# Optimization experiments

Hardware: AMD Instinct MI355X
Metric: run time of the kernel (lower is better)

Reference implementation:

```python
import jax, jax.numpy as jnp
import numpy as np
import math

SAMPLE_RATE = 16000
CUTOFF = 7500.0
Q = 0.707  # torchaudio default for lowpass_biquad

def _lowpass_biquad_coeffs(sample_rate, cutoff_freq, Q):
    w0 = 2.0 * math.pi * cutoff_freq / sample_rate
    alpha = math.sin(w0) / (2.0 * Q)
    cos_w0 = math.cos(w0)
    b0 = (1.0 - cos_w0) / 2.0
    b1 = 1.0 - cos_w0
    b2 = b0
    a0 = 1.0 + alpha
    a1 = -2.0 * cos_w0
    a2 = 1.0 - alpha
    # normalize by a0 (as torchaudio's biquad/lfilter does)
    return (b0 / a0, b1 / a0, b2 / a0, a1 / a0, a2 / a0)


def setup_inputs() -> dict:
    key = jax.random.key(0)
    x = jax.random.normal(key, (64, 320000), dtype=jnp.float32)
    return {"x": x}


def reference(x) -> jnp.ndarray:
    b0, b1, b2, a1, a2 = _lowpass_biquad_coeffs(SAMPLE_RATE, CUTOFF, Q)
    b0 = jnp.asarray(b0, x.dtype); b1 = jnp.asarray(b1, x.dtype)
    b2 = jnp.asarray(b2, x.dtype); a1 = jnp.asarray(a1, x.dtype)
    a2 = jnp.asarray(a2, x.dtype)

    B = x.shape[0]
    xT = jnp.swapaxes(x, 0, 1)  # [T, B] -> scan over time

    def step(carry, xn):
        x1, x2, y1, y2 = carry  # each [B]
        yn = b0 * xn + b1 * x1 + b2 * x2 - a1 * y1 - a2 * y2
        return (xn, x1, yn, y1), yn

    z = jnp.zeros((B,), x.dtype)
    _, yT = jax.lax.scan(step, (z, z, z, z), xT)
    return jnp.swapaxes(yT, 0, 1)  # [B, T]
```

## Files before the change

kernel.cpp:

```cpp
#include <hip/hip_runtime.h>
#include <cmath>

#ifndef M_PI
#define M_PI 3.14159265358979323846
#endif

constexpr int T_LEN  = 320000;
constexpr int B_ROWS = 64;
constexpr int CHUNK  = 32;
constexpr int VPT    = CHUNK / 4;
constexpr int NCHUNK = T_LEN / CHUNK;
constexpr int BLK_CHUNKS = 128;
constexpr int BLK_SPAN   = BLK_CHUNKS * CHUNK;
constexpr int HALO       = 3;
constexpr int HALO_VECS  = HALO * VPT;
constexpr int TILE_VECS  = HALO_VECS + BLK_CHUNKS * VPT;

__device__ __forceinline__ int swzv(int V) { return V ^ ((V >> 3) & 7); }

__global__ __launch_bounds__(256, 8) void biquad_combine_kernel(
    const float* __restrict__ x, float* __restrict__ y,
    float b0, float b1, float b2, float a1, float a2,
    float q30, float p30, float q31, float p31) {
  const int b   = blockIdx.x;
  const int row = blockIdx.y;
  const int t   = threadIdx.x;

  const int S       = b * BLK_SPAN;
  const int nchunks = min(BLK_CHUNKS, (T_LEN - S) / CHUNK);
  const int nvecs   = nchunks * VPT;

  const float* xr = x + (size_t)row * T_LEN;
  float*       yr = y + (size_t)row * T_LEN;

  __shared__ float4 tile[TILE_VECS];
  __shared__ float4 st[HALO + BLK_CHUNKS];

  if (b == 0) {
    const float4* src = reinterpret_cast<const float4*>(xr);
    for (int i = t; i < HALO_VECS + nvecs; i += 256)
      tile[swzv(i)] = (i < HALO_VECS) ? make_float4(0.f, 0.f, 0.f, 0.f)
                                      : src[i - HALO_VECS];
  } else {
    const float4* src = reinterpret_cast<const float4*>(xr + S - HALO * CHUNK);
    for (int i = t; i < HALO_VECS + nvecs; i += 256) tile[swzv(i)] = src[i];
  }
  __syncthreads();

  auto stepf = [&](float xn, float& X1, float& X2, float& Y1, float& Y2) -> float {
    float tt = fmaf(b2, X2, fmaf(b1, X1, b0 * xn));
    float u  = fmaf(-a2, Y2, tt);
    float yn = fmaf(-a1, Y1, u);
    X2 = X1; X1 = xn;
    Y2 = Y1; Y1 = yn;
    return yn;
  };

  if (t < HALO) {
    float4 h[VPT];
#pragma unroll
    for (int k = 0; k < VPT; ++k) h[k] = tile[swzv(t * VPT + k)];
    float hxl1 = h[VPT - 1].w, hxl2 = h[VPT - 1].z;
    float hx1 = 0.f, hx2 = 0.f, hy1 = 0.f, hy2 = 0.f;
#pragma unroll
    for (int k = 0; k < VPT; ++k) {
      stepf(h[k].x, hx1, hx2, hy1, hy2); stepf(h[k].y, hx1, hx2, hy1, hy2);
      stepf(h[k].z, hx1, hx2, hy1, hy2); stepf(h[k].w, hx1, hx2, hy1, hy2);
    }
    st[t] = make_float4(hy1, hy2, hxl1, hxl2);
  }

  const bool active = (t < nchunks);
  float4 m[VPT];
  const int vb = HALO_VECS + t * VPT;
  if (active) {
#pragma unroll
    for (int k = 0; k < VPT; ++k) m[k] = tile[swzv(vb + k)];
    float xl1 = m[VPT - 1].w, xl2 = m[VPT - 1].z;
    float x1 = 0.f, x2 = 0.f, y1 = 0.f, y2 = 0.f;
#pragma unroll
    for (int k = 0; k < VPT; ++k) {
      float4 v = m[k];
      m[k] = make_float4(stepf(v.x, x1, x2, y1, y2), stepf(v.y, x1, x2, y1, y2),
                         stepf(v.z, x1, x2, y1, y2), stepf(v.w, x1, x2, y1, y2));
    }
    st[HALO + t] = make_float4(y1, y2, xl1, xl2);
  }
  __syncthreads();

  if (active) {
    const int i = HALO + t;
    float4 sm3 = st[i - 3], sm2 = st[i - 2], sm1 = st[i - 1];
    float cA0 = fmaf(b1, sm3.z, fmaf(b2, sm3.w, fmaf(-a1, sm3.x, -a2 * sm3.y)));
    float cA1 = fmaf(-a1, cA0, fmaf(b2, sm3.z, -a2 * sm3.x));
    float yA1 = fmaf(q31, cA0, fmaf(p31, cA1, sm2.x));
    float yA2 = fmaf(q30, cA0, fmaf(p30, cA1, sm2.y));
    float cB0 = fmaf(b1, sm2.z, fmaf(b2, sm2.w, fmaf(-a1, yA1, -a2 * yA2)));
    float cB1 = fmaf(-a1, cB0, fmaf(b2, sm2.z, -a2 * yA1));
    float yB1 = fmaf(q31, cB0, fmaf(p31, cB1, sm1.x));
    float yB2 = fmaf(q30, cB0, fmaf(p30, cB1, sm1.y));
    float c0 = fmaf(b1, sm1.z, fmaf(b2, sm1.w, fmaf(-a1, yB1, -a2 * yB2)));
    float c1 = fmaf(-a1, c0, fmaf(b2, sm1.z, -a2 * yB1));
    float cm2, cm1;
    {
      m[0].x += c0; m[0].y += c1;
      float c2 = fmaf(-a1, c1, -a2 * c0); m[0].z += c2;
      float c3 = fmaf(-a1, c2, -a2 * c1); m[0].w += c3;
      cm2 = c2; cm1 = c3;
    }
#pragma unroll
    for (int k = 1; k < VPT; ++k) {
      float ca = fmaf(-a1, cm1, -a2 * cm2); m[k].x += ca;
      float cb = fmaf(-a1, ca, -a2 * cm1);  m[k].y += cb;
      float cc = fmaf(-a1, cb, -a2 * ca);   m[k].z += cc;
      float cd = fmaf(-a1, cc, -a2 * cb);   m[k].w += cd;
      cm2 = cc; cm1 = cd;
    }
#pragma unroll
    for (int k = 0; k < VPT; ++k) tile[swzv(vb + k)] = m[k];
  }
  __syncthreads();

  {
    float4* dst = reinterpret_cast<float4*>(yr + S);
    for (int i = t; i < nvecs; i += 256) dst[i] = tile[swzv(HALO_VECS + i)];
  }
}

extern "C" void kernel_launch(void* const* d_in, const int* in_sizes, int n_in,
                              void* d_out, int out_size, void* d_ws, size_t ws_size,
                              hipStream_t stream) {
  const float* x = (const float*)d_in[0];
  float*       y = (float*)d_out;

  const double sample_rate = 16000.0, cutoff = 7500.0, Q = 0.707;
  double w0    = 2.0 * M_PI * cutoff / sample_rate;
  double alpha = sin(w0) / (2.0 * Q);
  double cw    = cos(w0);
  double a0    = 1.0 + alpha;
  double b0d = ((1.0 - cw) * 0.5) / a0;
  double b1d = (1.0 - cw) / a0;
  double a1d = (-2.0 * cw) / a0;
  double a2d = (1.0 - alpha) / a0;

  double qm2 = 1.0, pm2 = 0.0, qm1 = 0.0, pm1 = 1.0;
  double q30 = 0, p30 = 0, q31 = 0, p31 = 0;
  for (int n = 2; n < CHUNK; ++n) {
    double qn = -a1d * qm1 - a2d * qm2;
    double pn = -a1d * pm1 - a2d * pm2;
    qm2 = qm1; pm2 = pm1; qm1 = qn; pm1 = pn;
    if (n == 30) { q30 = qn; p30 = pn; }
    if (n == 31) { q31 = qn; p31 = pn; }
  }

  dim3 block(256);
  dim3 grid((NCHUNK + BLK_CHUNKS - 1) / BLK_CHUNKS, B_ROWS);
  hipLaunchKernelGGL(biquad_combine_kernel, grid, block, 0, stream,
                     x, y, (float)b0d, (float)b1d, (float)b0d, (float)a1d, (float)a2d,
                     (float)q30, (float)p30, (float)q31, (float)p31);
}
```

Before: 33.71 us.

## Exchange chunk carry states via wavefront shuffles instead of shared memory

Each thread's end-of-chunk state (y1, y2, last two inputs) now reaches its neighbours through 64-lane shuffles rather than a shared-memory array and an extra block barrier. Every wavefront computes its own three-chunk halo so lane 0 can take its neighbours' state from broadcasts. The global load is unrolled into five register loads issued before any LDS store, and the occupancy hint in launch_bounds drops from 8 to 4. The intent is to remove a __syncthreads and LDS round-trips and to get more loads in flight. The cost is redundant halo work in every wave, and threads 128–255 now read LDS beyond the tile unguarded (only their stores are guarded).

```diff
diff --git a/kernel.cpp b/kernel.cpp
--- a/kernel.cpp
+++ b/kernel.cpp
@@ -18,32 +18,61 @@
 
 __device__ __forceinline__ int swzv(int V) { return V ^ ((V >> 3) & 7); }
 
-__global__ __launch_bounds__(256, 8) void biquad_combine_kernel(
+__device__ __forceinline__ float4 shfl_up4(float4 v, int d) {
+  float4 r;
+  r.x = __shfl_up(v.x, d); r.y = __shfl_up(v.y, d);
+  r.z = __shfl_up(v.z, d); r.w = __shfl_up(v.w, d);
+  return r;
+}
+__device__ __forceinline__ float4 bcast4(float4 v, int l) {
+  float4 r;
+  r.x = __shfl(v.x, l); r.y = __shfl(v.y, l);
+  r.z = __shfl(v.z, l); r.w = __shfl(v.w, l);
+  return r;
+}
+
+__global__ __launch_bounds__(256, 4) void biquad_shfl_kernel(
     const float* __restrict__ x, float* __restrict__ y,
     float b0, float b1, float b2, float a1, float a2,
     float q30, float p30, float q31, float p31) {
-  const int b   = blockIdx.x;
-  const int row = blockIdx.y;
-  const int t   = threadIdx.x;
+  const int b    = blockIdx.x;
+  const int row  = blockIdx.y;
+  const int t    = threadIdx.x;
+  const int lane = t & 63;
 
   const int S       = b * BLK_SPAN;
   const int nchunks = min(BLK_CHUNKS, (T_LEN - S) / CHUNK);
   const int nvecs   = nchunks * VPT;
+  const int ntot    = HALO_VECS + nvecs;
 
   const float* xr = x + (size_t)row * T_LEN;
   float*       yr = y + (size_t)row * T_LEN;
 
   __shared__ float4 tile[TILE_VECS];
-  __shared__ float4 st[HALO + BLK_CHUNKS];
-
-  if (b == 0) {
-    const float4* src = reinterpret_cast<const float4*>(xr);
-    for (int i = t; i < HALO_VECS + nvecs; i += 256)
-      tile[swzv(i)] = (i < HALO_VECS) ? make_float4(0.f, 0.f, 0.f, 0.f)
-                                      : src[i - HALO_VECS];
-  } else {
-    const float4* src = reinterpret_cast<const float4*>(xr + S - HALO * CHUNK);
-    for (int i = t; i < HALO_VECS + nvecs; i += 256) tile[swzv(i)] = src[i];
+
+  {
+    const float4 z4 = make_float4(0.f, 0.f, 0.f, 0.f);
+    float4 v0, v1, v2, v3, v4;
+    if (b == 0) {
+      const float4* g = reinterpret_cast<const float4*>(xr);
+      v0 = (t >= HALO_VECS && t < ntot) ? g[t - HALO_VECS] : z4;
+      v1 = (t + 256  < ntot) ? g[t + 256  - HALO_VECS] : z4;
+      v2 = (t + 512  < ntot) ? g[t + 512  - HALO_VECS] : z4;
+      v3 = (t + 768  < ntot) ? g[t + 768  - HALO_VECS] : z4;
+      v4 = (t + 1024 < ntot) ? g[t + 1024 - HALO_VECS] : z4;
+    } else {
+      const float4* g = reinterpret_cast<const float4*>(xr + S - HALO * CHUNK);
+      v0 = (t        < ntot) ? g[t]        : z4;
+      v1 = (t + 256  < ntot) ? g[t + 256]  : z4;
+      v2 = (t + 512  < ntot) ? g[t + 512]  : z4;
+      v3 = (t + 768  < ntot) ? g[t + 768]  : z4;
+      v4 = (t + 1024 < ntot) ? g[t + 1024] : z4;
+    }
+    if (t        < ntot) tile[swzv(t)]        = v0;
+    if (t + 256  < ntot) tile[swzv(t + 256)]  = v1;
+    if (t + 512  < ntot) tile[swzv(t + 512)]  = v2;
+    if (t + 768  < ntot) tile[swzv(t + 768)]  = v3;
+    if (t + 1024 < ntot) tile[swzv(t + 1024)] = v4;
   }
   __syncthreads();
 
@@ -56,27 +85,29 @@
     return yn;
   };
 
-  if (t < HALO) {
-    float4 h[VPT];
-#pragma unroll
-    for (int k = 0; k < VPT; ++k) h[k] = tile[swzv(t * VPT + k)];
-    float hxl1 = h[VPT - 1].w, hxl2 = h[VPT - 1].z;
-    float hx1 = 0.f, hx2 = 0.f, hy1 = 0.f, hy2 = 0.f;
-#pragma unroll
-    for (int k = 0; k < VPT; ++k) {
-      stepf(h[k].x, hx1, hx2, hy1, hy2); stepf(h[k].y, hx1, hx2, hy1, hy2);
-      stepf(h[k].z, hx1, hx2, hy1, hy2); stepf(h[k].w, hx1, hx2, hy1, hy2);
-    }
-    st[t] = make_float4(hy1, hy2, hxl1, hxl2);
-  }
-
-  const bool active = (t < nchunks);
+  float4 H = make_float4(0.f, 0.f, 0.f, 0.f);
+  if (lane < 3) {
+    const int hvb = HALO_VECS + ((t & ~63) - 3 + lane) * VPT;
+    float hx1 = 0.f, hx2 = 0.f, hy1 = 0.f, hy2 = 0.f, hxl1 = 0.f, hxl2 = 0.f;
+#pragma unroll
+    for (int g2 = 0; g2 < 4; ++g2) {
+      float4 ha = tile[swzv(hvb + 2 * g2)];
+      float4 hb = tile[swzv(hvb + 2 * g2 + 1)];
+      stepf(ha.x, hx1, hx2, hy1, hy2); stepf(ha.y, hx1, hx2, hy1, hy2);
+      stepf(ha.z, hx1, hx2, hy1, hy2); stepf(ha.w, hx1, hx2, hy1, hy2);
+      stepf(hb.x, hx1, hx2, hy1, hy2); stepf(hb.y, hx1, hx2, hy1, hy2);
+      stepf(hb.z, hx1, hx2, hy1, hy2); stepf(hb.w, hx1, hx2, hy1, hy2);
+      if (g2 == 3) { hxl1 = hb.w; hxl2 = hb.z; }
+    }
+    H = make_float4(hy1, hy2, hxl1, hxl2);
+  }
+
   float4 m[VPT];
   const int vb = HALO_VECS + t * VPT;
-  if (active) {
-#pragma unroll
-    for (int k = 0; k < VPT; ++k) m[k] = tile[swzv(vb + k)];
-    float xl1 = m[VPT - 1].w, xl2 = m[VPT - 1].z;
+#pragma unroll
+  for (int k = 0; k < VPT; ++k) m[k] = tile[swzv(vb + k)];
+  float xl1 = m[VPT - 1].w, xl2 = m[VPT - 1].z;
+  {
     float x1 = 0.f, x2 = 0.f, y1 = 0.f, y2 = 0.f;
 #pragma unroll
     for (int k = 0; k < VPT; ++k) {
@@ -84,13 +115,15 @@
       m[k] = make_float4(stepf(v.x, x1, x2, y1, y2), stepf(v.y, x1, x2, y1, y2),
                          stepf(v.z, x1, x2, y1, y2), stepf(v.w, x1, x2, y1, y2));
     }
-    st[HALO + t] = make_float4(y1, y2, xl1, xl2);
-  }
-  __syncthreads();
-
-  if (active) {
-    const int i = HALO + t;
-    float4 sm3 = st[i - 3], sm2 = st[i - 2], sm1 = st[i - 1];
+    float4 Sst = make_float4(y1, y2, xl1, xl2);
+    float4 up1 = shfl_up4(Sst, 1);
+    float4 up2 = shfl_up4(Sst, 2);
+    float4 up3 = shfl_up4(Sst, 3);
+    float4 H0 = bcast4(H, 0), H1 = bcast4(H, 1), H2 = bcast4(H, 2);
+    float4 sm1 = (lane == 0) ? H2 : up1;
+    float4 sm2 = (lane == 0) ? H1 : ((lane == 1) ? H2 : up2);
+    float4 sm3 = (lane == 0) ? H0 : ((lane == 1) ? H1 : ((lane == 2) ? H2 : up3));
+
     float cA0 = fmaf(b1, sm3.z, fmaf(b2, sm3.w, fmaf(-a1, sm3.x, -a2 * sm3.y)));
     float cA1 = fmaf(-a1, cA0, fmaf(b2, sm3.z, -a2 * sm3.x));
     float yA1 = fmaf(q31, cA0, fmaf(p31, cA1, sm2.x));
@@ -116,6 +149,8 @@
       float cd = fmaf(-a1, cc, -a2 * cb);   m[k].w += cd;
       cm2 = cc; cm1 = cd;
     }
+  }
+  if (t < nchunks) {
 #pragma unroll
     for (int k = 0; k < VPT; ++k) tile[swzv(vb + k)] = m[k];
   }
@@ -123,7 +158,11 @@
 
   {
     float4* dst = reinterpret_cast<float4*>(yr + S);
-    for (int i = t; i < nvecs; i += 256) dst[i] = tile[swzv(HALO_VECS + i)];
+#pragma unroll
+    for (int j = 0; j < 4; ++j) {
+      int i = t + 256 * j;
+      if (i < nvecs) dst[i] = tile[swzv(HALO_VECS + i)];
+    }
   }
 }
 
@@ -155,7 +194,7 @@
 
   dim3 block(256);
   dim3 grid((NCHUNK + BLK_CHUNKS - 1) / BLK_CHUNKS, B_ROWS);
-  hipLaunchKernelGGL(biquad_combine_kernel, grid, block, 0, stream,
+  hipLaunchKernelGGL(biquad_shfl_kernel, grid, block, 0, stream,
                      x, y, (float)b0d, (float)b1d, (float)b0d, (float)a1d, (float)a2d,
                      (float)q30, (float)p30, (float)q31, (float)p31);
 }
```

After: 34.47 us. +2.2%, slower.
